# Optimization experiments

Measured on AMD Instinct MI355X. Metric: run time of the kernel, lower is better.

The kernel has to match this reference:

```python
import jax, jax.numpy as jnp
import numpy as np

B, T, C = 4, 2048, 768
H, KVH, D = 6, 6, 128
HALF = D // 2


def setup_inputs() -> dict:
    key = jax.random.key(0)
    ks = jax.random.split(key, 5)
    x = jax.random.normal(ks[0], (B, T, C), dtype=jnp.float32)
    # true rotary frequencies
    inv_freq = 1.0 / (10000.0 ** (jnp.arange(HALF, dtype=jnp.float32) / HALF))
    ang = jnp.arange(T, dtype=jnp.float32)[:, None] * inv_freq[None, :]  # [T, HALF]
    cos, sin = jnp.cos(ang), jnp.sin(ang)
    s = 0.02
    wq = jax.random.normal(ks[1], (H * D, C), dtype=jnp.float32) * s
    wk = jax.random.normal(ks[2], (KVH * D, C), dtype=jnp.float32) * s
    wv = jax.random.normal(ks[3], (KVH * D, C), dtype=jnp.float32) * s
    wproj = jax.random.normal(ks[4], (C, C), dtype=jnp.float32) * s
    return {"x": x, "cos": cos, "sin": sin, "wq": wq, "wk": wk, "wv": wv, "wproj": wproj}


def _norm(t, eps=1e-6):
    # torch: (x - mean) / (std + eps), std unbiased (ddof=1)
    mean = jnp.mean(t, axis=-1, keepdims=True)
    var = jnp.sum((t - mean) ** 2, axis=-1, keepdims=True) / (t.shape[-1] - 1)
    return (t - mean) / (jnp.sqrt(var) + eps)


def _rope(t, cos, sin):
    # t: [B, T, heads, D]; cos/sin: [T, HALF]
    x1, x2 = t[..., :HALF], t[..., HALF:]
    c = cos[None, :, None, :]
    s = sin[None, :, None, :]
    return jnp.concatenate([x1 * c + x2 * s, -x1 * s + x2 * c], axis=-1)


def reference(x, cos, sin, wq, wk, wv, wproj):
    q = jnp.einsum('btc,oc->bto', x, wq).reshape(B, T, H, D)
    k = jnp.einsum('btc,oc->bto', x, wk).reshape(B, T, KVH, D)
    v = jnp.einsum('btc,oc->bto', x, wv).reshape(B, T, KVH, D)
    q = _norm(_rope(q, cos, sin))
    k = _norm(_rope(k, cos, sin))
    # -> [B, heads, T, D]
    q = q.transpose(0, 2, 1, 3)
    k = k.transpose(0, 2, 1, 3)
    v = v.transpose(0, 2, 1, 3)
    # nrep = H // KVH == 1, repeat_kv is a no-op here
    scale = 1.0 / jnp.sqrt(jnp.float32(D))
    scores = jnp.einsum('bhtd,bhsd->bhts', q, k) * scale  # [B,H,T,T]
    causal = jnp.tril(jnp.ones((T, T), dtype=bool))
    scores = jnp.where(causal[None, None], scores, jnp.float32(-1e30))
    attn = jax.nn.softmax(scores, axis=-1)
    y = jnp.einsum('bhts,bhsd->bhtd', attn, v)
    y = y.transpose(0, 2, 1, 3).reshape(B, T, H * D)
    return jnp.einsum('bto,co->btc', y, wproj)
```

## Files before the change

### kernel.cpp

```cpp
#include <hip/hip_runtime.h>

#define BB 4
#define TT 2048
#define CC 768
#define HH 6
#define DD 128
#define BT (BB * TT)
#define HALF 64
#define NBH (BB * HH)
#define QKSCALE 0.12753785627919282f

typedef __bf16 v8bf __attribute__((ext_vector_type(8)));
typedef float f32x4 __attribute__((ext_vector_type(4)));

__device__ __forceinline__ unsigned short f2b(float f) {
  union { float f; unsigned u; } v; v.f = f;
  unsigned r = v.u + 0x7FFFu + ((v.u >> 16) & 1u);
  return (unsigned short)(r >> 16);
}
__device__ __forceinline__ float b2f(unsigned short u) {
  union { unsigned u; float f; } v; v.u = (unsigned)u << 16;
  return v.f;
}
__device__ __forceinline__ unsigned pk2(float f0, float f1) {
  union { float f; unsigned u; } a, b; a.f = f1; b.f = f0;
  return __builtin_amdgcn_perm(a.u, b.u, 0x07060302u);
}

__device__ __forceinline__ void load_lds16(const void* g, void* l) {
  __builtin_amdgcn_global_load_lds(
      (const __attribute__((address_space(1))) unsigned int*)g,
      (__attribute__((address_space(3))) unsigned int*)(unsigned int)(unsigned long long)(l),
      16, 0, 0);
}

__global__ __launch_bounds__(256) void cvt_all_kernel(const float* __restrict__ x,
                                                      const float* __restrict__ w0,
                                                      const float* __restrict__ w1,
                                                      const float* __restrict__ w2,
                                                      const float* __restrict__ w3,
                                                      unsigned short* __restrict__ xb,
                                                      unsigned short* __restrict__ wb) {
  int bx = blockIdx.x;
  const float* src;
  unsigned short* dst;
  int i;
  if (bx < 6144) {
    src = x; dst = xb; i = bx * 256 + threadIdx.x;
  } else {
    int bsel = (bx - 6144) / 576;
    src = bsel == 0 ? w0 : bsel == 1 ? w1 : bsel == 2 ? w2 : w3;
    dst = wb + bsel * 589824;
    i = ((bx - 6144) % 576) * 256 + threadIdx.x;
  }
  float4 f = ((const float4*)src)[i];
  ushort4 o;
  o.x = f2b(f.x); o.y = f2b(f.y); o.z = f2b(f.z); o.w = f2b(f.w);
  ((ushort4*)dst)[i] = o;
}

__global__ __launch_bounds__(256) void gemm_qkv(const unsigned short* __restrict__ A,
                                                const unsigned short* __restrict__ Wall,
                                                unsigned short* __restrict__ qb,
                                                unsigned short* __restrict__ kb,
                                                unsigned short* __restrict__ vt) {
  __shared__ __align__(16) unsigned short As[2][512 * 8];
  __shared__ __align__(16) unsigned short Bs[2][512 * 8];
  const int m0 = blockIdx.x * 128;
  const int wsel = blockIdx.y / HH, h = blockIdx.y % HH;
  const unsigned short* W = Wall + (size_t)wsel * 589824 + (size_t)h * 128 * CC;
  const int tid = threadIdx.x;
  const int wave = tid >> 6, lane = tid & 63;
  const int fr = lane & 15, quad = lane >> 4;
  const int wm = (wave & 1) * 64, wn = (wave >> 1) * 64;

  f32x4 acc[4][4];
#pragma unroll
  for (int i = 0; i < 4; i++)
#pragma unroll
    for (int j = 0; j < 4; j++) acc[i][j] = (f32x4){0.f, 0.f, 0.f, 0.f};

  auto stage = [&](int kk, int buf) {
#pragma unroll
    for (int it = 0; it < 2; it++) {
      int base_slot = wave * 128 + it * 64;
      int sigma = base_slot + lane;
      int r = sigma >> 2, g = (sigma & 3) ^ ((r >> 1) & 3);
      load_lds16(A + (size_t)(m0 + r) * CC + kk + g * 8, &As[buf][base_slot * 8]);
      load_lds16(W + (size_t)r * CC + kk + g * 8, &Bs[buf][base_slot * 8]);
    }
  };

  stage(0, 0);
  __syncthreads();
  for (int step = 0; step < CC / 32; step++) {
    int buf = step & 1;
    if (step + 1 < CC / 32) stage((step + 1) * 32, buf ^ 1);
    v8bf af[4], bfr[4];
#pragma unroll
    for (int i = 0; i < 4; i++) {
      int ra = wm + i * 16 + fr;
      af[i] = *(const v8bf*)&As[buf][(4 * ra + (quad ^ ((ra >> 1) & 3))) * 8];
      int rb = wn + i * 16 + fr;
      bfr[i] = *(const v8bf*)&Bs[buf][(4 * rb + (quad ^ ((rb >> 1) & 3))) * 8];
    }
#pragma unroll
    for (int i = 0; i < 4; i++)
#pragma unroll
      for (int j = 0; j < 4; j++)
        acc[i][j] = __builtin_amdgcn_mfma_f32_16x16x32_bf16(af[i], bfr[j], acc[i][j], 0, 0, 0);
    __syncthreads();
  }

  if (wsel < 2) {
    unsigned short* dst = wsel ? kb : qb;
#pragma unroll
    for (int i = 0; i < 4; i++) {
      int rr0 = m0 + wm + i * 16 + quad * 4;
      int b = rr0 >> 11, t0 = rr0 & 2047;
      size_t base = ((size_t)(b * HH + h) * TT + t0) * DD;
#pragma unroll
      for (int j = 0; j < 4; j++) {
        int d = wn + j * 16 + fr;
#pragma unroll
        for (int r = 0; r < 4; r++)
          dst[base + (size_t)r * DD + d] = f2b(acc[i][j][r]);
      }
    }
  } else {
#pragma unroll
    for (int i = 0; i < 4; i++) {
      int rr0 = m0 + wm + i * 16 + quad * 4;
      int b = rr0 >> 11, t0 = rr0 & 2047;
      int bh = b * HH + h;
#pragma unroll
      for (int j = 0; j < 4; j++) {
        int d = wn + j * 16 + fr;
        ushort4 u = { f2b(acc[i][j][0]), f2b(acc[i][j][1]),
                      f2b(acc[i][j][2]), f2b(acc[i][j][3]) };
        *(ushort4*)&vt[((size_t)bh * DD + d) * TT + t0] = u;
      }
    }
  }
}

__global__ __launch_bounds__(256) void gemm_w64(const unsigned short* __restrict__ A,
                                                const unsigned short* __restrict__ W,
                                                float* __restrict__ C) {
  __shared__ __align__(16) unsigned short As[2][256 * 8];
  __shared__ __align__(16) unsigned short Bs[2][512 * 8];
  const int m0 = blockIdx.x * 64, n0 = blockIdx.y * 128;
  const int tid = threadIdx.x;
  const int wave = tid >> 6, lane = tid & 63;
  const int fr = lane & 15, quad = lane >> 4;
  const int wm = (wave & 1) * 32, wn = (wave >> 1) * 64;

  f32x4 acc[2][4];
#pragma unroll
  for (int i = 0; i < 2; i++)
#pragma unroll
    for (int j = 0; j < 4; j++) acc[i][j] = (f32x4){0.f, 0.f, 0.f, 0.f};

  auto stage = [&](int kk, int buf) {
    {
      int base_slot = wave * 64;
      int sigma = base_slot + lane;
      int r = sigma >> 2, g = (sigma & 3) ^ ((r >> 1) & 3);
      load_lds16(A + (size_t)(m0 + r) * CC + kk + g * 8, &As[buf][base_slot * 8]);
    }
#pragma unroll
    for (int it = 0; it < 2; it++) {
      int base_slot = wave * 128 + it * 64;
      int sigma = base_slot + lane;
      int r = sigma >> 2, g = (sigma & 3) ^ ((r >> 1) & 3);
      load_lds16(W + (size_t)(n0 + r) * CC + kk + g * 8, &Bs[buf][base_slot * 8]);
    }
  };

  stage(0, 0);
  __syncthreads();
  for (int step = 0; step < CC / 32; step++) {
    int buf = step & 1;
    if (step + 1 < CC / 32) stage((step + 1) * 32, buf ^ 1);
    v8bf af[2], bfr[4];
#pragma unroll
    for (int i = 0; i < 2; i++) {
      int ra = wm + i * 16 + fr;
      af[i] = *(const v8bf*)&As[buf][(4 * ra + (quad ^ ((ra >> 1) & 3))) * 8];
    }
#pragma unroll
    for (int j = 0; j < 4; j++) {
      int rb = wn + j * 16 + fr;
      bfr[j] = *(const v8bf*)&Bs[buf][(4 * rb + (quad ^ ((rb >> 1) & 3))) * 8];
    }
#pragma unroll
    for (int i = 0; i < 2; i++)
#pragma unroll
      for (int j = 0; j < 4; j++)
        acc[i][j] = __builtin_amdgcn_mfma_f32_16x16x32_bf16(af[i], bfr[j], acc[i][j], 0, 0, 0);
    __syncthreads();
  }

  const int orow = m0 + wm + quad * 4;
#pragma unroll
  for (int i = 0; i < 2; i++)
#pragma unroll
    for (int j = 0; j < 4; j++) {
      int oc = n0 + wn + j * 16 + fr;
#pragma unroll
      for (int r = 0; r < 4; r++)
        C[(size_t)(orow + i * 16 + r) * CC + oc] = acc[i][j][r];
    }
}

__global__ __launch_bounds__(256) void rope_all_kernel(unsigned short* __restrict__ qb,
                                                       unsigned short* __restrict__ kb,
                                                       const float* __restrict__ cosb,
                                                       const float* __restrict__ sinb) {
  int bx = blockIdx.x;
  unsigned short* qk = (bx < 12288) ? qb : kb;
  float scale = (bx < 12288) ? QKSCALE : 1.0f;
  int idx = (bx % 12288) * 4 + (threadIdx.x >> 6);
  int lane = threadIdx.x & 63;
  int tpos = idx & (TT - 1);
  size_t base = (size_t)idx * DD;

  float x1 = b2f(qk[base + lane]);
  float x2 = b2f(qk[base + HALF + lane]);
  float c = cosb[tpos * HALF + lane];
  float s = sinb[tpos * HALF + lane];
  float o1 = x1 * c + x2 * s;
  float o2 = x2 * c - x1 * s;

  float sum = o1 + o2;
#pragma unroll
  for (int off = 32; off; off >>= 1) sum += __shfl_xor(sum, off);
  float mean = sum * (1.f / 128.f);
  float d1 = o1 - mean, d2 = o2 - mean;
  float vs = d1 * d1 + d2 * d2;
#pragma unroll
  for (int off = 32; off; off >>= 1) vs += __shfl_xor(vs, off);
  float inv = scale / (sqrtf(vs * (1.f / 127.f)) + 1e-6f);

  qk[base + lane] = f2b(d1 * inv);
  qk[base + HALF + lane] = f2b(d2 * inv);
}

__global__ __launch_bounds__(256) void attn_mfma(const unsigned short* __restrict__ qtb,
                                                 const unsigned short* __restrict__ ktb,
                                                 const unsigned short* __restrict__ vtb,
                                                 unsigned short* __restrict__ Opart,
                                                 float* __restrict__ lpart) {
  __shared__ __align__(16) unsigned short Ks[2][512 * 8];
  __shared__ __align__(16) unsigned short Vts[2][512 * 8];
  __shared__ __align__(16) unsigned short Ps[4][32][40];

  const int u = blockIdx.x;
  const int bh = u % NBH;
  const int uu = u / NBH;
  int qt, c;
  if (uu < 16)      { qt = 15 - (uu >> 2); c = uu & 3; }
  else if (uu < 28) { int k = uu - 16; int q3 = k / 3; qt = 11 - q3; c = k - q3 * 3; }
  else if (uu < 36) { int k = uu - 28; qt = 7 - (k >> 1); c = k & 1; }
  else              { qt = 3 - (uu - 36); c = 0; }
  const int t0 = c * 16;
  const int t1 = min(t0 + 16, 4 * qt + 4);
  const int niter = t1 - t0;

  const int tid = threadIdx.x;
  const int wave = tid >> 6, lane = tid & 63;
  const int fr = lane & 15, quad = lane >> 4;
  const size_t head_base = (size_t)bh * TT * DD;
  const int m0 = qt * 128 + wave * 32;

  v8bf qf[2][4];
#pragma unroll
  for (int qs = 0; qs < 2; qs++)
#pragma unroll
    for (int kbk = 0; kbk < 4; kbk++)
      qf[qs][kbk] = *(const v8bf*)(qtb + head_base +
                                   (size_t)(m0 + qs * 16 + fr) * DD + kbk * 32 + quad * 8);

  const __bf16 one_bf = (__bf16)1.0f;
  v8bf ones = {one_bf, one_bf, one_bf, one_bf, one_bf, one_bf, one_bf, one_bf};

  f32x4 oacc[2][8];
#pragma unroll
  for (int qs = 0; qs < 2; qs++)
#pragma unroll
    for (int i = 0; i < 8; i++) oacc[qs][i] = (f32x4){0.f, 0.f, 0.f, 0.f};
  f32x4 lacc[2] = {(f32x4){0.f, 0.f, 0.f, 0.f}, (f32x4){0.f, 0.f, 0.f, 0.f}};

  auto stage = [&](int jt, int buf) {
    const unsigned short* kbase = ktb + head_base + (size_t)(jt * 32) * DD;
    const unsigned short* vbase = vtb + head_base + jt * 32;
#pragma unroll
    for (int it = 0; it < 2; it++) {
      int base_slot = it * 256 + wave * 64;
      int sigma = base_slot + lane;
      int s = sigma >> 4, gk = (sigma & 15) ^ (s & 7);
      load_lds16(kbase + (size_t)s * DD + gk * 8, &Ks[buf][base_slot * 8]);
      int d = sigma >> 2, gv = (sigma & 3) ^ ((d >> 1) & 3);
      load_lds16(vbase + (size_t)d * TT + gv * 8, &Vts[buf][base_slot * 8]);
    }
  };

  stage(t0, 0);
  __syncthreads();

  for (int it = 0; it < niter; it++) {
    const int jt = t0 + it;
    const int buf = it & 1;
    if (it + 1 < niter) stage(jt + 1, buf ^ 1);

    const int j0 = jt * 32;
    if (j0 <= m0 + 31) {
      f32x4 st[2][2];
#pragma unroll
      for (int qs = 0; qs < 2; qs++) { st[qs][0] = (f32x4){0,0,0,0}; st[qs][1] = (f32x4){0,0,0,0}; }
#pragma unroll
      for (int kbk = 0; kbk < 4; kbk++) {
        int g = 4 * kbk + quad;
        v8bf a0 = *(const v8bf*)&Ks[buf][(16 * fr + (g ^ (fr & 7))) * 8];
        v8bf a1 = *(const v8bf*)&Ks[buf][(16 * (fr + 16) + (g ^ (fr & 7))) * 8];
        st[0][0] = __builtin_amdgcn_mfma_f32_16x16x32_bf16(a0, qf[0][kbk], st[0][0], 0, 0, 0);
        st[0][1] = __builtin_amdgcn_mfma_f32_16x16x32_bf16(a1, qf[0][kbk], st[0][1], 0, 0, 0);
        st[1][0] = __builtin_amdgcn_mfma_f32_16x16x32_bf16(a0, qf[1][kbk], st[1][0], 0, 0, 0);
        st[1][1] = __builtin_amdgcn_mfma_f32_16x16x32_bf16(a1, qf[1][kbk], st[1][1], 0, 0, 0);
      }

      const bool diag = (j0 + 31 > m0);
#pragma unroll
      for (int qs = 0; qs < 2; qs++) {
        float p[8];
        if (diag) {
          const int qrow = m0 + qs * 16 + fr;
#pragma unroll
          for (int r = 0; r < 4; r++) {
            int c0 = j0 + quad * 4 + r;
            p[r]     = (c0      <= qrow) ? exp2f(st[qs][0][r]) : 0.f;
            p[4 + r] = (c0 + 16 <= qrow) ? exp2f(st[qs][1][r]) : 0.f;
          }
        } else {
#pragma unroll
          for (int r = 0; r < 4; r++) { p[r] = exp2f(st[qs][0][r]); p[4 + r] = exp2f(st[qs][1][r]); }
        }
        uint2 w0 = { pk2(p[0], p[1]), pk2(p[2], p[3]) };
        uint2 w1 = { pk2(p[4], p[5]), pk2(p[6], p[7]) };
        *(uint2*)&Ps[wave][qs * 16 + fr][quad * 4] = w0;
        *(uint2*)&Ps[wave][qs * 16 + fr][16 + quad * 4] = w1;
      }

      v8bf pa0 = *(const v8bf*)&Ps[wave][fr][quad * 8];
      v8bf pa1 = *(const v8bf*)&Ps[wave][16 + fr][quad * 8];
#pragma unroll
      for (int nt2 = 0; nt2 < 8; nt2++) {
        int d = nt2 * 16 + fr;
        v8bf vb = *(const v8bf*)&Vts[buf][(4 * d + (quad ^ ((d >> 1) & 3))) * 8];
        oacc[0][nt2] = __builtin_amdgcn_mfma_f32_16x16x32_bf16(pa0, vb, oacc[0][nt2], 0, 0, 0);
        oacc[1][nt2] = __builtin_amdgcn_mfma_f32_16x16x32_bf16(pa1, vb, oacc[1][nt2], 0, 0, 0);
      }
      lacc[0] = __builtin_amdgcn_mfma_f32_16x16x32_bf16(pa0, ones, lacc[0], 0, 0, 0);
      lacc[1] = __builtin_amdgcn_mfma_f32_16x16x32_bf16(pa1, ones, lacc[1], 0, 0, 0);
    }
    __syncthreads();
  }

  unsigned short* Oc = Opart + (size_t)c * (NBH * TT * DD) + head_base;
#pragma unroll
  for (int qs = 0; qs < 2; qs++) {
#pragma unroll
    for (int nt2 = 0; nt2 < 8; nt2++)
#pragma unroll
      for (int r = 0; r < 4; r++)
        Oc[(size_t)(m0 + qs * 16 + quad * 4 + r) * DD + nt2 * 16 + fr] = f2b(oacc[qs][nt2][r]);
    if (fr == 0) {
#pragma unroll
      for (int r = 0; r < 4; r++)
        lpart[c * (NBH * TT) + bh * TT + m0 + qs * 16 + quad * 4 + r] = lacc[qs][r];
    }
  }
}

__global__ __launch_bounds__(256) void combine_kernel(const unsigned short* __restrict__ Opart,
                                                      const float* __restrict__ lpart,
                                                      unsigned short* __restrict__ yb) {
  int idx = blockIdx.x * 256 + threadIdx.x;
  int row = idx >> 5;
  int dg = (idx & 31) * 4;
  int t = row & 2047;
  int qt = t >> 7;
  int nc = (4 * qt + 4 + 15) >> 4;

  float a0 = 0.f, a1 = 0.f, a2 = 0.f, a3 = 0.f, l = 0.f;
  for (int cchunk = 0; cchunk < nc; cchunk++) {
    ushort4 o = *(const ushort4*)&Opart[(size_t)cchunk * (NBH * TT * DD) + (size_t)row * DD + dg];
    a0 += b2f(o.x); a1 += b2f(o.y); a2 += b2f(o.z); a3 += b2f(o.w);
    l += lpart[cchunk * (NBH * TT) + row];
  }
  float linv = 1.f / l;
  int bh = row >> 11;
  int b = bh / HH, h = bh % HH;
  ushort4 u = { f2b(a0 * linv), f2b(a1 * linv), f2b(a2 * linv), f2b(a3 * linv) };
  *(ushort4*)&yb[((size_t)(b * TT + t)) * CC + h * DD + dg] = u;
}

extern "C" void kernel_launch(void* const* d_in, const int* in_sizes, int n_in,
                              void* d_out, int out_size, void* d_ws, size_t ws_size,
                              hipStream_t stream) {
  const float* x     = (const float*)d_in[0];
  const float* cosb  = (const float*)d_in[1];
  const float* sinb  = (const float*)d_in[2];
  const float* wq    = (const float*)d_in[3];
  const float* wk    = (const float*)d_in[4];
  const float* wv    = (const float*)d_in[5];
  const float* wproj = (const float*)d_in[6];
  float* out = (float*)d_out;

  char* w = (char*)d_ws;
  unsigned short* q_t   = (unsigned short*)(w);
  unsigned short* k_t   = (unsigned short*)(w + 12582912);
  unsigned short* v_t   = (unsigned short*)(w + 25165824);
  unsigned short* yb    = (unsigned short*)(w + 37748736);
  unsigned short* xb    = (unsigned short*)(w + 50331648);
  float*          lpart = (float*)(w + 50331648);
  unsigned short* wb    = (unsigned short*)(w + 62914560);
  unsigned short* Opart = (unsigned short*)(w + 67633152);

  cvt_all_kernel<<<8448, 256, 0, stream>>>(x, wq, wk, wv, wproj, xb, wb);

  gemm_qkv<<<dim3(BT / 128, 3 * HH), 256, 0, stream>>>(xb, wb, q_t, k_t, v_t);

  rope_all_kernel<<<24576, 256, 0, stream>>>(q_t, k_t, cosb, sinb);

  attn_mfma<<<960, 256, 0, stream>>>(q_t, k_t, v_t, Opart, lpart);
  combine_kernel<<<6144, 256, 0, stream>>>(Opart, lpart, yb);

  gemm_w64<<<dim3(BT / 64, CC / 128), 256, 0, stream>>>(yb, wb + 3 * 589824, out);
}
```

Before: 245.6 us.

## Make attention kernel persistent with atomic work-queue and MFMA priority hints

```diff
diff --git a/kernel.cpp b/kernel.cpp
--- a/kernel.cpp
+++ b/kernel.cpp
@@ -8,6 +8,7 @@
 #define BT (BB * TT)
 #define HALF 64
 #define NBH (BB * HH)
+#define NCHUNK 960
 #define QKSCALE 0.12753785627919282f
 
 typedef __bf16 v8bf __attribute__((ext_vector_type(8)));
@@ -216,8 +217,10 @@
 __global__ __launch_bounds__(256) void rope_all_kernel(unsigned short* __restrict__ qb,
                                                        unsigned short* __restrict__ kb,
                                                        const float* __restrict__ cosb,
-                                                       const float* __restrict__ sinb) {
+                                                       const float* __restrict__ sinb,
+                                                       unsigned int* __restrict__ ctr) {
   int bx = blockIdx.x;
+  if (bx == 0 && threadIdx.x == 0) *ctr = 0u;
   unsigned short* qk = (bx < 12288) ? qb : kb;
   float scale = (bx < 12288) ? QKSCALE : 1.0f;
   int idx = (bx % 12288) * 4 + (threadIdx.x >> 6);
@@ -250,134 +253,147 @@
                                                  const unsigned short* __restrict__ ktb,
                                                  const unsigned short* __restrict__ vtb,
                                                  unsigned short* __restrict__ Opart,
-                                                 float* __restrict__ lpart) {
+                                                 float* __restrict__ lpart,
+                                                 unsigned int* __restrict__ ctr) {
   __shared__ __align__(16) unsigned short Ks[2][512 * 8];
   __shared__ __align__(16) unsigned short Vts[2][512 * 8];
   __shared__ __align__(16) unsigned short Ps[4][32][40];
-
-  const int u = blockIdx.x;
-  const int bh = u % NBH;
-  const int uu = u / NBH;
-  int qt, c;
-  if (uu < 16)      { qt = 15 - (uu >> 2); c = uu & 3; }
-  else if (uu < 28) { int k = uu - 16; int q3 = k / 3; qt = 11 - q3; c = k - q3 * 3; }
-  else if (uu < 36) { int k = uu - 28; qt = 7 - (k >> 1); c = k & 1; }
-  else              { qt = 3 - (uu - 36); c = 0; }
-  const int t0 = c * 16;
-  const int t1 = min(t0 + 16, 4 * qt + 4);
-  const int niter = t1 - t0;
+  __shared__ unsigned int s_u;
 
   const int tid = threadIdx.x;
   const int wave = tid >> 6, lane = tid & 63;
   const int fr = lane & 15, quad = lane >> 4;
-  const size_t head_base = (size_t)bh * TT * DD;
-  const int m0 = qt * 128 + wave * 32;
-
-  v8bf qf[2][4];
-#pragma unroll
-  for (int qs = 0; qs < 2; qs++)
-#pragma unroll
-    for (int kbk = 0; kbk < 4; kbk++)
-      qf[qs][kbk] = *(const v8bf*)(qtb + head_base +
-                                   (size_t)(m0 + qs * 16 + fr) * DD + kbk * 32 + quad * 8);
 
   const __bf16 one_bf = (__bf16)1.0f;
-  v8bf ones = {one_bf, one_bf, one_bf, one_bf, one_bf, one_bf, one_bf, one_bf};
-
-  f32x4 oacc[2][8];
-#pragma unroll
-  for (int qs = 0; qs < 2; qs++)
-#pragma unroll
-    for (int i = 0; i < 8; i++) oacc[qs][i] = (f32x4){0.f, 0.f, 0.f, 0.f};
-  f32x4 lacc[2] = {(f32x4){0.f, 0.f, 0.f, 0.f}, (f32x4){0.f, 0.f, 0.f, 0.f}};
-
-  auto stage = [&](int jt, int buf) {
-    const unsigned short* kbase = ktb + head_base + (size_t)(jt * 32) * DD;
-    const unsigned short* vbase = vtb + head_base + jt * 32;
-#pragma unroll
-    for (int it = 0; it < 2; it++) {
-      int base_slot = it * 256 + wave * 64;
-      int sigma = base_slot + lane;
-      int s = sigma >> 4, gk = (sigma & 15) ^ (s & 7);
-      load_lds16(kbase + (size_t)s * DD + gk * 8, &Ks[buf][base_slot * 8]);
-      int d = sigma >> 2, gv = (sigma & 3) ^ ((d >> 1) & 3);
-      load_lds16(vbase + (size_t)d * TT + gv * 8, &Vts[buf][base_slot * 8]);
-    }
-  };
-
-  stage(t0, 0);
-  __syncthreads();
-
-  for (int it = 0; it < niter; it++) {
-    const int jt = t0 + it;
-    const int buf = it & 1;
-    if (it + 1 < niter) stage(jt + 1, buf ^ 1);
-
-    const int j0 = jt * 32;
-    if (j0 <= m0 + 31) {
-      f32x4 st[2][2];
-#pragma unroll
-      for (int qs = 0; qs < 2; qs++) { st[qs][0] = (f32x4){0,0,0,0}; st[qs][1] = (f32x4){0,0,0,0}; }
-#pragma unroll
-      for (int kbk = 0; kbk < 4; kbk++) {
-        int g = 4 * kbk + quad;
-        v8bf a0 = *(const v8bf*)&Ks[buf][(16 * fr + (g ^ (fr & 7))) * 8];
-        v8bf a1 = *(const v8bf*)&Ks[buf][(16 * (fr + 16) + (g ^ (fr & 7))) * 8];
-        st[0][0] = __builtin_amdgcn_mfma_f32_16x16x32_bf16(a0, qf[0][kbk], st[0][0], 0, 0, 0);
-        st[0][1] = __builtin_amdgcn_mfma_f32_16x16x32_bf16(a1, qf[0][kbk], st[0][1], 0, 0, 0);
-        st[1][0] = __builtin_amdgcn_mfma_f32_16x16x32_bf16(a0, qf[1][kbk], st[1][0], 0, 0, 0);
-        st[1][1] = __builtin_amdgcn_mfma_f32_16x16x32_bf16(a1, qf[1][kbk], st[1][1], 0, 0, 0);
+  const v8bf ones = {one_bf, one_bf, one_bf, one_bf, one_bf, one_bf, one_bf, one_bf};
+
+  for (;;) {
+    if (tid == 0) s_u = atomicAdd(ctr, 1u);
+    __syncthreads();
+    const unsigned u = s_u;
+    if (u >= NCHUNK) break;
+
+    const int bh = u % NBH;
+    const int uu = u / NBH;
+    int qt, c;
+    if (uu < 16)      { qt = 15 - (uu >> 2); c = uu & 3; }
+    else if (uu < 28) { int k = uu - 16; int q3 = k / 3; qt = 11 - q3; c = k - q3 * 3; }
+    else if (uu < 36) { int k = uu - 28; qt = 7 - ((k >> 1)); c = k & 1; }
+    else              { qt = 3 - (uu - 36); c = 0; }
+    const int t0 = c * 16;
+    const int t1 = min(t0 + 16, 4 * qt + 4);
+    const int niter = t1 - t0;
+
+    const size_t head_base = (size_t)bh * TT * DD;
+    const int m0 = qt * 128 + wave * 32;
+
+    v8bf qf[2][4];
+#pragma unroll
+    for (int qs = 0; qs < 2; qs++)
+#pragma unroll
+      for (int kbk = 0; kbk < 4; kbk++)
+        qf[qs][kbk] = *(const v8bf*)(qtb + head_base +
+                                     (size_t)(m0 + qs * 16 + fr) * DD + kbk * 32 + quad * 8);
+
+    f32x4 oacc[2][8];
+#pragma unroll
+    for (int qs = 0; qs < 2; qs++)
+#pragma unroll
+      for (int i = 0; i < 8; i++) oacc[qs][i] = (f32x4){0.f, 0.f, 0.f, 0.f};
+    f32x4 lacc[2] = {(f32x4){0.f, 0.f, 0.f, 0.f}, (f32x4){0.f, 0.f, 0.f, 0.f}};
+
+    auto stage = [&](int jt, int buf) {
+      const unsigned short* kbase = ktb + head_base + (size_t)(jt * 32) * DD;
+      const unsigned short* vbase = vtb + head_base + jt * 32;
+#pragma unroll
+      for (int it = 0; it < 2; it++) {
+        int base_slot = it * 256 + wave * 64;
+        int sigma = base_slot + lane;
+        int s = sigma >> 4, gk = (sigma & 15) ^ (s & 7);
+        load_lds16(kbase + (size_t)s * DD + gk * 8, &Ks[buf][base_slot * 8]);
+        int d = sigma >> 2, gv = (sigma & 3) ^ ((d >> 1) & 3);
+        load_lds16(vbase + (size_t)d * TT + gv * 8, &Vts[buf][base_slot * 8]);
       }
-
-      const bool diag = (j0 + 31 > m0);
-#pragma unroll
-      for (int qs = 0; qs < 2; qs++) {
-        float p[8];
-        if (diag) {
-          const int qrow = m0 + qs * 16 + fr;
-#pragma unroll
-          for (int r = 0; r < 4; r++) {
-            int c0 = j0 + quad * 4 + r;
-            p[r]     = (c0      <= qrow) ? exp2f(st[qs][0][r]) : 0.f;
-            p[4 + r] = (c0 + 16 <= qrow) ? exp2f(st[qs][1][r]) : 0.f;
+    };
+
+    stage(t0, 0);
+    __syncthreads();
+
+    for (int it = 0; it < niter; it++) {
+      const int jt = t0 + it;
+      const int buf = it & 1;
+      if (it + 1 < niter) stage(jt + 1, buf ^ 1);
+
+      const int j0 = jt * 32;
+      if (j0 <= m0 + 31) {
+        f32x4 st[2][2];
+#pragma unroll
+        for (int qs = 0; qs < 2; qs++) { st[qs][0] = (f32x4){0,0,0,0}; st[qs][1] = (f32x4){0,0,0,0}; }
+        __builtin_amdgcn_s_setprio(1);
+#pragma unroll
+        for (int kbk = 0; kbk < 4; kbk++) {
+          int g = 4 * kbk + quad;
+          v8bf a0 = *(const v8bf*)&Ks[buf][(16 * fr + (g ^ (fr & 7))) * 8];
+          v8bf a1 = *(const v8bf*)&Ks[buf][(16 * (fr + 16) + (g ^ (fr & 7))) * 8];
+          st[0][0] = __builtin_amdgcn_mfma_f32_16x16x32_bf16(a0, qf[0][kbk], st[0][0], 0, 0, 0);
+          st[0][1] = __builtin_amdgcn_mfma_f32_16x16x32_bf16(a1, qf[0][kbk], st[0][1], 0, 0, 0);
+          st[1][0] = __builtin_amdgcn_mfma_f32_16x16x32_bf16(a0, qf[1][kbk], st[1][0], 0, 0, 0);
+          st[1][1] = __builtin_amdgcn_mfma_f32_16x16x32_bf16(a1, qf[1][kbk], st[1][1], 0, 0, 0);
+        }
+        __builtin_amdgcn_s_setprio(0);
+
+        const bool diag = (j0 + 31 > m0);
+#pragma unroll
+        for (int qs = 0; qs < 2; qs++) {
+          float p[8];
+          if (diag) {
+            const int qrow = m0 + qs * 16 + fr;
+#pragma unroll
+            for (int r = 0; r < 4; r++) {
+              int c0 = j0 + quad * 4 + r;
+              p[r]     = (c0      <= qrow) ? exp2f(st[qs][0][r]) : 0.f;
+              p[4 + r] = (c0 + 16 <= qrow) ? exp2f(st[qs][1][r]) : 0.f;
+            }
+          } else {
+#pragma unroll
+            for (int r = 0; r < 4; r++) { p[r] = exp2f(st[qs][0][r]); p[4 + r] = exp2f(st[qs][1][r]); }
           }
-        } else {
-#pragma unroll
-          for (int r = 0; r < 4; r++) { p[r] = exp2f(st[qs][0][r]); p[4 + r] = exp2f(st[qs][1][r]); }
+          uint2 w0 = { pk2(p[0], p[1]), pk2(p[2], p[3]) };
+          uint2 w1 = { pk2(p[4], p[5]), pk2(p[6], p[7]) };
+          *(uint2*)&Ps[wave][qs * 16 + fr][quad * 4] = w0;
+          *(uint2*)&Ps[wave][qs * 16 + fr][16 + quad * 4] = w1;
         }
-        uint2 w0 = { pk2(p[0], p[1]), pk2(p[2], p[3]) };
-        uint2 w1 = { pk2(p[4], p[5]), pk2(p[6], p[7]) };
-        *(uint2*)&Ps[wave][qs * 16 + fr][quad * 4] = w0;
-        *(uint2*)&Ps[wave][qs * 16 + fr][16 + quad * 4] = w1;
+
+        v8bf pa0 = *(const v8bf*)&Ps[wave][fr][quad * 8];
+        v8bf pa1 = *(const v8bf*)&Ps[wave][16 + fr][quad * 8];
+        __builtin_amdgcn_s_setprio(1);
+#pragma unroll
+        for (int nt2 = 0; nt2 < 8; nt2++) {
+          int d = nt2 * 16 + fr;
+          v8bf vb = *(const v8bf*)&Vts[buf][(4 * d + (quad ^ ((d >> 1) & 3))) * 8];
+          oacc[0][nt2] = __builtin_amdgcn_mfma_f32_16x16x32_bf16(pa0, vb, oacc[0][nt2], 0, 0, 0);
+          oacc[1][nt2] = __builtin_amdgcn_mfma_f32_16x16x32_bf16(pa1, vb, oacc[1][nt2], 0, 0, 0);
+        }
+        lacc[0] = __builtin_amdgcn_mfma_f32_16x16x32_bf16(pa0, ones, lacc[0], 0, 0, 0);
+        lacc[1] = __builtin_amdgcn_mfma_f32_16x16x32_bf16(pa1, ones, lacc[1], 0, 0, 0);
+        __builtin_amdgcn_s_setprio(0);
       }
-
-      v8bf pa0 = *(const v8bf*)&Ps[wave][fr][quad * 8];
-      v8bf pa1 = *(const v8bf*)&Ps[wave][16 + fr][quad * 8];
-#pragma unroll
-      for (int nt2 = 0; nt2 < 8; nt2++) {
-        int d = nt2 * 16 + fr;
-        v8bf vb = *(const v8bf*)&Vts[buf][(4 * d + (quad ^ ((d >> 1) & 3))) * 8];
-        oacc[0][nt2] = __builtin_amdgcn_mfma_f32_16x16x32_bf16(pa0, vb, oacc[0][nt2], 0, 0, 0);
-        oacc[1][nt2] = __builtin_amdgcn_mfma_f32_16x16x32_bf16(pa1, vb, oacc[1][nt2], 0, 0, 0);
+      __syncthreads();
+    }
+
+    unsigned short* Oc = Opart + (size_t)c * (NBH * TT * DD) + head_base;
+#pragma unroll
+    for (int qs = 0; qs < 2; qs++) {
+#pragma unroll
+      for (int nt2 = 0; nt2 < 8; nt2++)
+#pragma unroll
+        for (int r = 0; r < 4; r++)
+          Oc[(size_t)(m0 + qs * 16 + quad * 4 + r) * DD + nt2 * 16 + fr] = f2b(oacc[qs][nt2][r]);
+      if (fr == 0) {
+#pragma unroll
+        for (int r = 0; r < 4; r++)
+          lpart[c * (NBH * TT) + bh * TT + m0 + qs * 16 + quad * 4 + r] = lacc[qs][r];
       }
-      lacc[0] = __builtin_amdgcn_mfma_f32_16x16x32_bf16(pa0, ones, lacc[0], 0, 0, 0);
-      lacc[1] = __builtin_amdgcn_mfma_f32_16x16x32_bf16(pa1, ones, lacc[1], 0, 0, 0);
-    }
-    __syncthreads();
-  }
-
-  unsigned short* Oc = Opart + (size_t)c * (NBH * TT * DD) + head_base;
-#pragma unroll
-  for (int qs = 0; qs < 2; qs++) {
-#pragma unroll
-    for (int nt2 = 0; nt2 < 8; nt2++)
-#pragma unroll
-      for (int r = 0; r < 4; r++)
-        Oc[(size_t)(m0 + qs * 16 + quad * 4 + r) * DD + nt2 * 16 + fr] = f2b(oacc[qs][nt2][r]);
-    if (fr == 0) {
-#pragma unroll
-      for (int r = 0; r < 4; r++)
-        lpart[c * (NBH * TT) + bh * TT + m0 + qs * 16 + quad * 4 + r] = lacc[qs][r];
     }
   }
 }
@@ -401,8 +417,8 @@
   float linv = 1.f / l;
   int bh = row >> 11;
   int b = bh / HH, h = bh % HH;
-  ushort4 u = { f2b(a0 * linv), f2b(a1 * linv), f2b(a2 * linv), f2b(a3 * linv) };
-  *(ushort4*)&yb[((size_t)(b * TT + t)) * CC + h * DD + dg] = u;
+  ushort4 uo = { f2b(a0 * linv), f2b(a1 * linv), f2b(a2 * linv), f2b(a3 * linv) };
+  *(ushort4*)&yb[((size_t)(b * TT + t)) * CC + h * DD + dg] = uo;
 }
 
 extern "C" void kernel_launch(void* const* d_in, const int* in_sizes, int n_in,
@@ -422,6 +438,7 @@
   unsigned short* k_t   = (unsigned short*)(w + 12582912);
   unsigned short* v_t   = (unsigned short*)(w + 25165824);
   unsigned short* yb    = (unsigned short*)(w + 37748736);
+  unsigned int*   ctr   = (unsigned int*)(w + 37748736);
   unsigned short* xb    = (unsigned short*)(w + 50331648);
   float*          lpart = (float*)(w + 50331648);
   unsigned short* wb    = (unsigned short*)(w + 62914560);
@@ -431,9 +448,9 @@
 
   gemm_qkv<<<dim3(BT / 128, 3 * HH), 256, 0, stream>>>(xb, wb, q_t, k_t, v_t);
 
-  rope_all_kernel<<<24576, 256, 0, stream>>>(q_t, k_t, cosb, sinb);
-
-  attn_mfma<<<960, 256, 0, stream>>>(q_t, k_t, v_t, Opart, lpart);
+  rope_all_kernel<<<24576, 256, 0, stream>>>(q_t, k_t, cosb, sinb, ctr);
+
+  attn_mfma<<<768, 256, 0, stream>>>(q_t, k_t, v_t, Opart, lpart, ctr);
   combine_kernel<<<6144, 256, 0, stream>>>(Opart, lpart, yb);
 
   gemm_w64<<<dim3(BT / 64, CC / 128), 256, 0, stream>>>(yb, wb + 3 * 589824, out);
```

Result: slower. 252.0 us (+2.6%).

## Route attention P tile through ds_bpermute instead of LDS, add setprio and occupancy bound

Applied to the files above, without the earlier changes.

```diff
diff --git a/kernel.cpp b/kernel.cpp
--- a/kernel.cpp
+++ b/kernel.cpp
@@ -246,14 +246,13 @@
   qk[base + HALF + lane] = f2b(d2 * inv);
 }
 
-__global__ __launch_bounds__(256) void attn_mfma(const unsigned short* __restrict__ qtb,
-                                                 const unsigned short* __restrict__ ktb,
-                                                 const unsigned short* __restrict__ vtb,
-                                                 unsigned short* __restrict__ Opart,
-                                                 float* __restrict__ lpart) {
+__global__ __launch_bounds__(256, 4) void attn_mfma(const unsigned short* __restrict__ qtb,
+                                                    const unsigned short* __restrict__ ktb,
+                                                    const unsigned short* __restrict__ vtb,
+                                                    unsigned short* __restrict__ Opart,
+                                                    float* __restrict__ lpart) {
   __shared__ __align__(16) unsigned short Ks[2][512 * 8];
   __shared__ __align__(16) unsigned short Vts[2][512 * 8];
-  __shared__ __align__(16) unsigned short Ps[4][32][40];
 
   const int u = blockIdx.x;
   const int bh = u % NBH;
@@ -270,6 +269,8 @@
   const int tid = threadIdx.x;
   const int wave = tid >> 6, lane = tid & 63;
   const int fr = lane & 15, quad = lane >> 4;
+  const int idxf = 4 * ((quad & 1) * 32 + fr);
+  const int idxs = idxf + 64;
   const size_t head_base = (size_t)bh * TT * DD;
   const int m0 = qt * 128 + wave * 32;
 
@@ -318,6 +319,7 @@
       f32x4 st[2][2];
 #pragma unroll
       for (int qs = 0; qs < 2; qs++) { st[qs][0] = (f32x4){0,0,0,0}; st[qs][1] = (f32x4){0,0,0,0}; }
+      __builtin_amdgcn_s_setprio(1);
 #pragma unroll
       for (int kbk = 0; kbk < 4; kbk++) {
         int g = 4 * kbk + quad;
@@ -328,8 +330,10 @@
         st[1][0] = __builtin_amdgcn_mfma_f32_16x16x32_bf16(a0, qf[1][kbk], st[1][0], 0, 0, 0);
         st[1][1] = __builtin_amdgcn_mfma_f32_16x16x32_bf16(a1, qf[1][kbk], st[1][1], 0, 0, 0);
       }
+      __builtin_amdgcn_s_setprio(0);
 
       const bool diag = (j0 + 31 > m0);
+      v8bf pa0, pa1;
 #pragma unroll
       for (int qs = 0; qs < 2; qs++) {
         float p[8];
@@ -345,14 +349,26 @@
 #pragma unroll
           for (int r = 0; r < 4; r++) { p[r] = exp2f(st[qs][0][r]); p[4 + r] = exp2f(st[qs][1][r]); }
         }
-        uint2 w0 = { pk2(p[0], p[1]), pk2(p[2], p[3]) };
-        uint2 w1 = { pk2(p[4], p[5]), pk2(p[6], p[7]) };
-        *(uint2*)&Ps[wave][qs * 16 + fr][quad * 4] = w0;
-        *(uint2*)&Ps[wave][qs * 16 + fr][16 + quad * 4] = w1;
+        unsigned A0 = pk2(p[0], p[1]), A1 = pk2(p[2], p[3]);
+        unsigned B0 = pk2(p[4], p[5]), B1 = pk2(p[6], p[7]);
+        unsigned alo0 = (unsigned)__builtin_amdgcn_ds_bpermute(idxf, (int)A0);
+        unsigned alo1 = (unsigned)__builtin_amdgcn_ds_bpermute(idxf, (int)A1);
+        unsigned ahi0 = (unsigned)__builtin_amdgcn_ds_bpermute(idxs, (int)A0);
+        unsigned ahi1 = (unsigned)__builtin_amdgcn_ds_bpermute(idxs, (int)A1);
+        unsigned blo0 = (unsigned)__builtin_amdgcn_ds_bpermute(idxf, (int)B0);
+        unsigned blo1 = (unsigned)__builtin_amdgcn_ds_bpermute(idxf, (int)B1);
+        unsigned bhi0 = (unsigned)__builtin_amdgcn_ds_bpermute(idxs, (int)B0);
+        unsigned bhi1 = (unsigned)__builtin_amdgcn_ds_bpermute(idxs, (int)B1);
+        const bool ql = (quad < 2);
+        union { unsigned w[4]; v8bf v; } pa;
+        pa.w[0] = ql ? alo0 : blo0;
+        pa.w[1] = ql ? alo1 : blo1;
+        pa.w[2] = ql ? ahi0 : bhi0;
+        pa.w[3] = ql ? ahi1 : bhi1;
+        if (qs == 0) pa0 = pa.v; else pa1 = pa.v;
       }
 
-      v8bf pa0 = *(const v8bf*)&Ps[wave][fr][quad * 8];
-      v8bf pa1 = *(const v8bf*)&Ps[wave][16 + fr][quad * 8];
+      __builtin_amdgcn_s_setprio(1);
 #pragma unroll
       for (int nt2 = 0; nt2 < 8; nt2++) {
         int d = nt2 * 16 + fr;
@@ -362,6 +378,7 @@
       }
       lacc[0] = __builtin_amdgcn_mfma_f32_16x16x32_bf16(pa0, ones, lacc[0], 0, 0, 0);
       lacc[1] = __builtin_amdgcn_mfma_f32_16x16x32_bf16(pa1, ones, lacc[1], 0, 0, 0);
+      __builtin_amdgcn_s_setprio(0);
     }
     __syncthreads();
   }
@@ -401,8 +418,8 @@
   float linv = 1.f / l;
   int bh = row >> 11;
   int b = bh / HH, h = bh % HH;
-  ushort4 u = { f2b(a0 * linv), f2b(a1 * linv), f2b(a2 * linv), f2b(a3 * linv) };
-  *(ushort4*)&yb[((size_t)(b * TT + t)) * CC + h * DD + dg] = u;
+  ushort4 uo = { f2b(a0 * linv), f2b(a1 * linv), f2b(a2 * linv), f2b(a3 * linv) };
+  *(ushort4*)&yb[((size_t)(b * TT + t)) * CC + h * DD + dg] = uo;
 }
 
 extern "C" void kernel_launch(void* const* d_in, const int* in_sizes, int n_in,
```

Measured after the change: 288.5 us. +17.5%, slower.
